# Kernel tuning notes

Measured on AMD Instinct MI355X. Metric: run time of the kernel, lower is better.

## Reference

```python
import jax, jax.numpy as jnp
import numpy as np

N = 4096          # nodes
IN_DIM = 256
OUT_DIM = 128
EDGE_DIM = 64
N_SAMPLE = 128
N_EDGES = 65536   # undirected edges (edge ids 1..N_EDGES; id 0 = no edge)
ALPHA = 0.2       # leaky-relu negative slope


def _glorot(key, shape):
    fan_in, fan_out = shape[0], shape[-1]
    scale = 1.414 * np.sqrt(2.0 / (fan_in + fan_out))
    return jax.random.normal(key, shape, jnp.float32) * scale


def setup_inputs() -> dict:
    rng = np.random.default_rng(0)
    # sample unique undirected edges (i < j); np.unique sorts lexicographically,
    # which matches torch's row-major e_index.nonzero() ordering, so assigning
    # sequential ids 1..n here makes edges == arange(1, n+1) in the update step.
    ii = rng.integers(0, N, size=3 * N_EDGES)
    jj = rng.integers(0, N, size=3 * N_EDGES)
    lo, hi = np.minimum(ii, jj), np.maximum(ii, jj)
    ok = lo < hi
    pairs = np.unique(np.stack([lo[ok], hi[ok]], axis=1), axis=0)[:N_EDGES]
    n = pairs.shape[0]
    ids = np.arange(1, n + 1, dtype=np.int32)
    e_index = np.zeros((N, N), np.int32)
    e_index[pairs[:, 0], pairs[:, 1]] = ids
    e_index[pairs[:, 1], pairs[:, 0]] = ids
    # per-node neighbor sampling with replacement (hoisted from torch forward)
    neigh = np.empty((N, N_SAMPLE), np.int32)
    for v in range(N):
        nz = np.nonzero(e_index[v])[0]
        neigh[v] = v if nz.size == 0 else rng.choice(nz, N_SAMPLE)

    key = jax.random.key(0)
    ks = jax.random.split(key, 8)
    return {
        "features": jax.random.normal(ks[0], (N, IN_DIM), jnp.float32),
        "e_index": jnp.asarray(e_index),
        "neigh": jnp.asarray(neigh),
        "to_update": jnp.asarray(pairs.astype(np.int32)),
        "emb": jax.random.normal(ks[1], (n + 1, EDGE_DIM), jnp.float32),
        "W": _glorot(ks[2], (IN_DIM, OUT_DIM)),
        "W2": _glorot(ks[3], (OUT_DIM, EDGE_DIM)),
        "W3": _glorot(ks[4], (EDGE_DIM, EDGE_DIM)),
        "B": _glorot(ks[5], (1, EDGE_DIM)),
        "a": _glorot(ks[6], (2 * OUT_DIM + EDGE_DIM, 1)),
    }


def reference(features, e_index, neigh, to_update, emb, W, W2, W3, B, a):
    x = features @ W                                        # [N, OUT]
    xn = x[neigh]                                           # [N, S, OUT] gather
    eid = jnp.take_along_axis(e_index, neigh, axis=1)       # [N, S] edge ids
    en = emb[eid]                                           # [N, S, ED] gather
    a_input = jnp.concatenate(
        [jnp.broadcast_to(x[:, None, :], xn.shape), xn, en], axis=2
    )                                                       # [N, S, 2*OUT+ED]
    e = jax.nn.leaky_relu((a_input @ a)[..., 0], ALPHA)     # [N, S]
    att = jax.nn.softmax(e, axis=1)                         # dropout = id (eval)
    h_prime = jnp.einsum('ns,nsd->nd', att, xn)             # [N, OUT]
    output = jax.nn.elu(h_prime + x)
    # edge update: (output[i] + output[j]) @ W2 == matmul(output[pair], W2).sum(1)
    edges = e_index[to_update[:, 0], to_update[:, 1]]       # == 1..n
    v_input = (output[to_update[:, 0]] + output[to_update[:, 1]]) @ W2
    e_input = emb[edges] @ W3
    a_in2 = jnp.concatenate([B, e_input + v_input + B], axis=0)  # [n+1, ED]
    emb_new = jax.nn.relu(a_in2 * emb)
    return output, emb_new
```

## Files before the change

### kernel.cpp

```cpp
#include <hip/hip_runtime.h>
#include <hip/hip_bf16.h>

#define N_NODES 4096
#define IN_DIM  256
#define OUT_DIM 128
#define EDGE_DIM 64
#define N_SAMPLE 128

__device__ __forceinline__ float wsum64(float v) {
#pragma unroll
  for (int off = 32; off; off >>= 1) v += __shfl_xor(v, off, 64);
  return v;
}
__device__ __forceinline__ float wmax64(float v) {
#pragma unroll
  for (int off = 32; off; off >>= 1) v = fmaxf(v, __shfl_xor(v, off, 64));
  return v;
}

__global__ void __launch_bounds__(128) gemm_x_kernel(const float* __restrict__ feat,
                                                     const float* __restrict__ W,
                                                     float* __restrict__ x) {
  const int t  = threadIdx.x;
  const int v0 = blockIdx.x * 8;
  __shared__ float f[8][IN_DIM];
  float* fflat = &f[0][0];
  for (int idx = t; idx < 8 * IN_DIM; idx += 128)
    fflat[idx] = feat[v0 * IN_DIM + idx];
  __syncthreads();
  float acc[8] = {0.f, 0.f, 0.f, 0.f, 0.f, 0.f, 0.f, 0.f};
  for (int i = 0; i < IN_DIM; i += 4) {
    const float w0 = W[(i + 0) * OUT_DIM + t];
    const float w1 = W[(i + 1) * OUT_DIM + t];
    const float w2 = W[(i + 2) * OUT_DIM + t];
    const float w3 = W[(i + 3) * OUT_DIM + t];
#pragma unroll
    for (int r = 0; r < 8; ++r) {
      const float4 fv = *reinterpret_cast<const float4*>(&f[r][i]);
      acc[r] += fv.x * w0 + fv.y * w1 + fv.z * w2 + fv.w * w3;
    }
  }
#pragma unroll
  for (int r = 0; r < 8; ++r) x[(v0 + r) * OUT_DIM + t] = acc[r];
}

__global__ void __launch_bounds__(64) s12_kernel(const float* __restrict__ x,
                                                 const float* __restrict__ a,
                                                 float* __restrict__ s1,
                                                 float* __restrict__ s2) {
  const int v = blockIdx.x, l = threadIdx.x;
  const float x0 = x[v * OUT_DIM + l], x1 = x[v * OUT_DIM + 64 + l];
  float c1 = x0 * a[l] + x1 * a[64 + l];
  float c2 = x0 * a[OUT_DIM + l] + x1 * a[OUT_DIM + 64 + l];
  c1 = wsum64(c1);
  c2 = wsum64(c2);
  if (l == 0) { s1[v] = c1; s2[v] = c2; }
}

__global__ void __launch_bounds__(256) s3_kernel(const float* __restrict__ emb,
                                                 const float* __restrict__ a,
                                                 float* __restrict__ s3, int rows) {
  const int w = threadIdx.x >> 6, l = threadIdx.x & 63;
  const int r = blockIdx.x * 4 + w;
  if (r >= rows) return;
  float c = emb[r * EDGE_DIM + l] * a[2 * OUT_DIM + l];
  c = wsum64(c);
  if (l == 0) s3[r] = c;
}

__global__ void __launch_bounds__(64) attn_kernel(const float* __restrict__ x,
                                                  const float* __restrict__ s1,
                                                  const float* __restrict__ s2,
                                                  const float* __restrict__ s3,
                                                  const int* __restrict__ neigh,
                                                  const int* __restrict__ eidx,
                                                  float* __restrict__ out) {
  const int v = blockIdx.x;
  const int t = threadIdx.x;
  __shared__ float att[N_SAMPLE];
  __shared__ int   us[N_SAMPLE];

  const int u0 = neigh[v * N_SAMPLE + t];
  const int u1 = neigh[v * N_SAMPLE + 64 + t];
  us[t]      = u0;
  us[t + 64] = u1;
  const float s1v = s1[v];
  float e0 = s1v + s2[u0] + s3[eidx[v * N_NODES + u0]];
  float e1 = s1v + s2[u1] + s3[eidx[v * N_NODES + u1]];
  e0 = e0 > 0.f ? e0 : 0.2f * e0;
  e1 = e1 > 0.f ? e1 : 0.2f * e1;
  const float m = wmax64(fmaxf(e0, e1));
  const float p0 = __expf(e0 - m), p1 = __expf(e1 - m);
  const float inv = 1.0f / wsum64(p0 + p1);
  att[t]      = p0;
  att[t + 64] = p1;
  __syncthreads();

  float2 h = make_float2(0.f, 0.f);
#pragma unroll 8
  for (int s = 0; s < N_SAMPLE; ++s) {
    const float a = att[s];
    const float2 xv = *reinterpret_cast<const float2*>(&x[us[s] * OUT_DIM + 2 * t]);
    h.x += a * xv.x;
    h.y += a * xv.y;
  }
  const float2 xs = *reinterpret_cast<const float2*>(&x[v * OUT_DIM + 2 * t]);
  float ox = h.x * inv + xs.x;
  float oy = h.y * inv + xs.y;
  ox = ox > 0.f ? ox : expm1f(ox);
  oy = oy > 0.f ? oy : expm1f(oy);
  float2 r = make_float2(ox, oy);
  *reinterpret_cast<float2*>(&out[v * OUT_DIM + 2 * t]) = r;
}

__global__ void __launch_bounds__(256) y_kernel(const float* __restrict__ out,
                                                const float* __restrict__ W2,
                                                float* __restrict__ Y) {
  const int t  = threadIdx.x;
  const int r0 = blockIdx.x * 16;
  __shared__ float o[16][132];
  for (int idx = t; idx < 16 * OUT_DIM; idx += 256)
    o[idx >> 7][idx & 127] = out[r0 * OUT_DIM + idx];
  __syncthreads();
  const int r  = t >> 4;
  const int c0 = (t & 15) * 4;
  float4 acc = make_float4(0.f, 0.f, 0.f, 0.f);
  for (int k = 0; k < OUT_DIM; k += 4) {
#pragma unroll
    for (int kk = 0; kk < 4; ++kk) {
      const float av = o[r][k + kk];
      const float4 w = *reinterpret_cast<const float4*>(&W2[(k + kk) * EDGE_DIM + c0]);
      acc.x += av * w.x; acc.y += av * w.y; acc.z += av * w.z; acc.w += av * w.w;
    }
  }
  *reinterpret_cast<float4*>(&Y[(r0 + r) * EDGE_DIM + c0]) = acc;
}

#define TE 64
__global__ void __launch_bounds__(256) edge_fused_kernel(const float* __restrict__ Y,
                                                         const float* __restrict__ emb,
                                                         const int* __restrict__ eidx,
                                                         const int* __restrict__ tu,
                                                         const float* __restrict__ W3,
                                                         const float* __restrict__ Bv,
                                                         float* __restrict__ emb_new, int n) {
  const int t  = threadIdx.x;
  const int k0 = blockIdx.x * TE;
  __shared__ float Ain[TE][68];
  __shared__ int   tus[2 * TE];

  if (t < 2 * TE) {
    const int idx = 2 * k0 + t;
    tus[t] = (idx < 2 * n) ? tu[idx] : 0;
  }
  {
    const int e  = t >> 2, q = t & 3;
    const int ke = k0 + e;
    if (ke < n) {
      const int i = tu[2 * ke], j = tu[2 * ke + 1];
      const int id = eidx[i * N_NODES + j];
#pragma unroll
      for (int kk = 0; kk < 16; kk += 4) {
        const int k = q * 16 + kk;
        *reinterpret_cast<float4*>(&Ain[e][k]) =
            *reinterpret_cast<const float4*>(&emb[id * EDGE_DIM + k]);
      }
    }
  }
  __syncthreads();

  const int e0 = (t >> 4) * 4;
  const int c0 = (t & 15) * 4;
  const float4 b4 = *reinterpret_cast<const float4*>(&Bv[c0]);
  float4 acc[4];
#pragma unroll
  for (int m = 0; m < 4; ++m) acc[m] = b4;

#pragma unroll 4
  for (int k = 0; k < EDGE_DIM; k += 4) {
    float4 a[4];
#pragma unroll
    for (int m = 0; m < 4; ++m) a[m] = *reinterpret_cast<const float4*>(&Ain[e0 + m][k]);
#pragma unroll
    for (int kk = 0; kk < 4; ++kk) {
      const float4 w = *reinterpret_cast<const float4*>(&W3[(k + kk) * EDGE_DIM + c0]);
#pragma unroll
      for (int m = 0; m < 4; ++m) {
        const float av = reinterpret_cast<const float*>(&a[m])[kk];
        acc[m].x += av * w.x; acc[m].y += av * w.y; acc[m].z += av * w.z; acc[m].w += av * w.w;
      }
    }
  }

#pragma unroll
  for (int m = 0; m < 4; ++m) {
    const int ke = k0 + e0 + m;
    if (ke < n) {
      const int i = tus[2 * (e0 + m)], j = tus[2 * (e0 + m) + 1];
      const float4 yi = *reinterpret_cast<const float4*>(&Y[i * EDGE_DIM + c0]);
      const float4 yj = *reinterpret_cast<const float4*>(&Y[j * EDGE_DIM + c0]);
      const float4 ek = *reinterpret_cast<const float4*>(&emb[(ke + 1) * EDGE_DIM + c0]);
      float4 r;
      r.x = fmaxf((acc[m].x + yi.x + yj.x) * ek.x, 0.f);
      r.y = fmaxf((acc[m].y + yi.y + yj.y) * ek.y, 0.f);
      r.z = fmaxf((acc[m].z + yi.z + yj.z) * ek.z, 0.f);
      r.w = fmaxf((acc[m].w + yi.w + yj.w) * ek.w, 0.f);
      *reinterpret_cast<float4*>(&emb_new[(ke + 1) * EDGE_DIM + c0]) = r;
    }
  }
  if (blockIdx.x == 0 && t < 16) {
    const int cc = t * 4;
    const float4 b0 = *reinterpret_cast<const float4*>(&Bv[cc]);
    const float4 e0v = *reinterpret_cast<const float4*>(&emb[cc]);
    float4 r;
    r.x = fmaxf(b0.x * e0v.x, 0.f);
    r.y = fmaxf(b0.y * e0v.y, 0.f);
    r.z = fmaxf(b0.z * e0v.z, 0.f);
    r.w = fmaxf(b0.w * e0v.w, 0.f);
    *reinterpret_cast<float4*>(&emb_new[cc]) = r;
  }
}

extern "C" void kernel_launch(void* const* d_in, const int* in_sizes, int n_in,
                              void* d_out, int out_size, void* d_ws, size_t ws_size,
                              hipStream_t stream) {
  const float* feat  = (const float*)d_in[0];
  const int*   eidx  = (const int*)d_in[1];
  const int*   neigh = (const int*)d_in[2];
  const int*   tu    = (const int*)d_in[3];
  const float* emb   = (const float*)d_in[4];
  const float* W     = (const float*)d_in[5];
  const float* W2    = (const float*)d_in[6];
  const float* W3    = (const float*)d_in[7];
  const float* Bv    = (const float*)d_in[8];
  const float* a     = (const float*)d_in[9];
  const int n    = in_sizes[3] / 2;
  const int rows = in_sizes[4] / EDGE_DIM;

  float* x  = (float*)d_ws;
  float* s1 = x + N_NODES * OUT_DIM;
  float* s2 = s1 + N_NODES;
  float* s3 = s2 + N_NODES;
  float* Y  = s3 + ((rows + 3) & ~3);

  float* out_nodes = (float*)d_out;
  float* emb_new   = out_nodes + N_NODES * OUT_DIM;

  hipLaunchKernelGGL(gemm_x_kernel, dim3(N_NODES / 8), dim3(128), 0, stream, feat, W, x);
  hipLaunchKernelGGL(s12_kernel, dim3(N_NODES), dim3(64), 0, stream, x, a, s1, s2);
  hipLaunchKernelGGL(s3_kernel, dim3((rows + 3) / 4), dim3(256), 0, stream, emb, a, s3, rows);
  hipLaunchKernelGGL(attn_kernel, dim3(N_NODES), dim3(64), 0, stream,
                     x, s1, s2, s3, neigh, eidx, out_nodes);
  hipLaunchKernelGGL(y_kernel, dim3(N_NODES / 16), dim3(256), 0, stream,
                     out_nodes, W2, Y);
  hipLaunchKernelGGL(edge_fused_kernel, dim3((n + TE - 1) / TE), dim3(256), 0, stream,
                     Y, emb, eidx, tu, W3, Bv, emb_new, n);
}
```

Before: 198.0 us.

## Split attention aggregation over four waves per node with shared-memory reduction

The attention kernel now runs 256 threads (four wavefronts) per node instead of one wavefront. Each wave accumulates a quarter of the 128 sampled neighbors, and the partial sums are reduced through shared memory. The softmax is computed by two waves with a cross-wave max and sum reduction. The aim is more memory-level parallelism for the gathered neighbor rows, at the cost of extra barriers and idle threads during the softmax and final reduction.

```diff
diff --git a/kernel.cpp b/kernel.cpp
--- a/kernel.cpp
+++ b/kernel.cpp
@@ -68,49 +68,66 @@
   if (l == 0) s3[r] = c;
 }
 
-__global__ void __launch_bounds__(64) attn_kernel(const float* __restrict__ x,
-                                                  const float* __restrict__ s1,
-                                                  const float* __restrict__ s2,
-                                                  const float* __restrict__ s3,
-                                                  const int* __restrict__ neigh,
-                                                  const int* __restrict__ eidx,
-                                                  float* __restrict__ out) {
+__global__ void __launch_bounds__(256) attn_kernel(const float* __restrict__ x,
+                                                   const float* __restrict__ s1,
+                                                   const float* __restrict__ s2,
+                                                   const float* __restrict__ s3,
+                                                   const int* __restrict__ neigh,
+                                                   const int* __restrict__ eidx,
+                                                   float* __restrict__ out) {
   const int v = blockIdx.x;
   const int t = threadIdx.x;
+  const int w = t >> 6, l = t & 63;
   __shared__ float att[N_SAMPLE];
   __shared__ int   us[N_SAMPLE];
-
-  const int u0 = neigh[v * N_SAMPLE + t];
-  const int u1 = neigh[v * N_SAMPLE + 64 + t];
-  us[t]      = u0;
-  us[t + 64] = u1;
-  const float s1v = s1[v];
-  float e0 = s1v + s2[u0] + s3[eidx[v * N_NODES + u0]];
-  float e1 = s1v + s2[u1] + s3[eidx[v * N_NODES + u1]];
-  e0 = e0 > 0.f ? e0 : 0.2f * e0;
-  e1 = e1 > 0.f ? e1 : 0.2f * e1;
-  const float m = wmax64(fmaxf(e0, e1));
-  const float p0 = __expf(e0 - m), p1 = __expf(e1 - m);
-  const float inv = 1.0f / wsum64(p0 + p1);
-  att[t]      = p0;
-  att[t + 64] = p1;
-  __syncthreads();
+  __shared__ float red[4];
+  __shared__ float2 hpart[4][64];
+
+  if (t < N_SAMPLE) {
+    const int u = neigh[v * N_SAMPLE + t];
+    us[t] = u;
+    float e = s1[v] + s2[u] + s3[eidx[v * N_NODES + u]];
+    e = e > 0.f ? e : 0.2f * e;
+    att[t] = e;
+    const float m = wmax64(e);
+    if (l == 0) red[w] = m;
+  }
+  __syncthreads();
+  const float m = fmaxf(red[0], red[1]);
+  if (t < N_SAMPLE) {
+    const float p = __expf(att[t] - m);
+    att[t] = p;
+    const float s = wsum64(p);
+    if (l == 0) red[2 + w] = s;
+  }
+  __syncthreads();
+  const float inv = 1.0f / (red[2] + red[3]);
 
   float2 h = make_float2(0.f, 0.f);
+  const int s0 = w * 32;
 #pragma unroll 8
-  for (int s = 0; s < N_SAMPLE; ++s) {
+  for (int s = s0; s < s0 + 32; ++s) {
     const float a = att[s];
-    const float2 xv = *reinterpret_cast<const float2*>(&x[us[s] * OUT_DIM + 2 * t]);
+    const float2 xv = *reinterpret_cast<const float2*>(&x[us[s] * OUT_DIM + 2 * l]);
     h.x += a * xv.x;
     h.y += a * xv.y;
   }
-  const float2 xs = *reinterpret_cast<const float2*>(&x[v * OUT_DIM + 2 * t]);
-  float ox = h.x * inv + xs.x;
-  float oy = h.y * inv + xs.y;
-  ox = ox > 0.f ? ox : expm1f(ox);
-  oy = oy > 0.f ? oy : expm1f(oy);
-  float2 r = make_float2(ox, oy);
-  *reinterpret_cast<float2*>(&out[v * OUT_DIM + 2 * t]) = r;
+  hpart[w][l] = h;
+  __syncthreads();
+
+  if (t < 64) {
+    float2 H = hpart[0][t];
+    const float2 p1 = hpart[1][t], p2 = hpart[2][t], p3 = hpart[3][t];
+    H.x += p1.x + p2.x + p3.x;
+    H.y += p1.y + p2.y + p3.y;
+    const float2 xs = *reinterpret_cast<const float2*>(&x[v * OUT_DIM + 2 * t]);
+    float ox = H.x * inv + xs.x;
+    float oy = H.y * inv + xs.y;
+    ox = ox > 0.f ? ox : expm1f(ox);
+    oy = oy > 0.f ? oy : expm1f(oy);
+    float2 r = make_float2(ox, oy);
+    *reinterpret_cast<float2*>(&out[v * OUT_DIM + 2 * t]) = r;
+  }
 }
 
 __global__ void __launch_bounds__(256) y_kernel(const float* __restrict__ out,
@@ -249,7 +266,7 @@
   hipLaunchKernelGGL(gemm_x_kernel, dim3(N_NODES / 8), dim3(128), 0, stream, feat, W, x);
   hipLaunchKernelGGL(s12_kernel, dim3(N_NODES), dim3(64), 0, stream, x, a, s1, s2);
   hipLaunchKernelGGL(s3_kernel, dim3((rows + 3) / 4), dim3(256), 0, stream, emb, a, s3, rows);
-  hipLaunchKernelGGL(attn_kernel, dim3(N_NODES), dim3(64), 0, stream,
+  hipLaunchKernelGGL(attn_kernel, dim3(N_NODES), dim3(256), 0, stream,
                      x, s1, s2, s3, neigh, eidx, out_nodes);
   hipLaunchKernelGGL(y_kernel, dim3(N_NODES / 16), dim3(256), 0, stream,
                      out_nodes, W2, Y);
```

After: 199.7 us. About the same (+0.8%).
